# Performance work log

Hardware: AMD Instinct MI355X
Metric: run time of the kernel (lower is better)

The kernel has to match this reference:

```python
import jax, jax.numpy as jnp
import numpy as np

Q_HEADS, KV_HEADS, HEAD_SIZE, H, MAX_LEN = 16, 4, 64, 1024, 4096
B, S = 1, 4096


def _rope_tables(max_len, head_size):
    half = head_size // 2
    inv_freq = 1.0 / (10000.0 ** (np.arange(half, dtype=np.float32) / half))
    pos = np.arange(max_len, dtype=np.float32)
    ang = pos[:, None] * inv_freq[None, :]  # [max_len, half]
    return jnp.asarray(np.sin(ang)), jnp.asarray(np.cos(ang))


def setup_inputs() -> dict:
    key = jax.random.key(0)
    ks = jax.random.split(key, 6)
    sc = 1.0 / np.sqrt(H)
    x = jax.random.normal(ks[0], (B, S, H), dtype=jnp.float32)
    wq = jax.random.normal(ks[1], (H, H), dtype=jnp.float32) * sc
    wk = jax.random.normal(ks[2], (H, KV_HEADS * HEAD_SIZE), dtype=jnp.float32) * sc
    wv = jax.random.normal(ks[3], (H, KV_HEADS * HEAD_SIZE), dtype=jnp.float32) * sc
    wo = jax.random.normal(ks[4], (H, H), dtype=jnp.float32) * sc
    sin, cos = _rope_tables(MAX_LEN, HEAD_SIZE)
    full_mask = jnp.tril(jnp.ones((MAX_LEN, MAX_LEN), dtype=bool))
    attention_mask = jnp.ones((B, S), dtype=jnp.int32)
    return {"x": x, "attention_mask": attention_mask, "start": 0,
            "wq": wq, "wk": wk, "wv": wv, "wo": wo,
            "sin": sin, "cos": cos, "full_mask": full_mask}


def _rotate(t, sin, cos, start):
    # t: [b, heads, s, head_size]; interleaved even/odd RoPE
    s = t.shape[2]
    sn = sin[start:start + s, :][None, None, :, :]
    cs = cos[start:start + s, :][None, None, :, :]
    even, odd = t[..., 0::2], t[..., 1::2]
    out_even = cs * even - sn * odd
    out_odd = sn * even + cs * odd
    return jnp.stack((out_even, out_odd), axis=-1).reshape(t.shape)


def _expand_kv(t, group):
    # [b, kv_heads, s, d] -> [b, kv_heads*group, s, d]
    b, kvh, s, d = t.shape
    return jnp.broadcast_to(t[:, :, None], (b, kvh, group, s, d)).reshape(b, kvh * group, s, d)


def reference(x, attention_mask, start, wq, wk, wv, wo, sin, cos, full_mask):
    b, s, _ = x.shape
    group = Q_HEADS // KV_HEADS
    Q = (x @ wq).reshape(b, s, Q_HEADS, HEAD_SIZE).transpose(0, 2, 1, 3)
    K = (x @ wk).reshape(b, s, KV_HEADS, HEAD_SIZE).transpose(0, 2, 1, 3)
    V = (x @ wv).reshape(b, s, KV_HEADS, HEAD_SIZE).transpose(0, 2, 1, 3)
    Q = _rotate(Q, sin, cos, start)
    K = _rotate(K, sin, cos, start)
    K = _expand_kv(K, group)
    V = _expand_kv(V, group)
    z = jnp.einsum('bhqd,bhkd->bhqk', Q, K) / (HEAD_SIZE ** 0.5)
    kv_len = start + s
    mask = full_mask[:s, :kv_len][None, None, :, :]
    amask = (attention_mask[:, :kv_len] != 0)[:, None, None, :]
    mask = mask & amask
    z = jnp.where(mask, z, -1000000.0)
    A = jax.nn.softmax(z, axis=-1)
    ctx = jnp.einsum('bhqk,bhkd->bhqd', A, V)
    q_mask = attention_mask[:, :s].astype(ctx.dtype)[:, None, :, None]
    ctx = ctx * q_mask
    ctx = ctx.transpose(0, 2, 1, 3).reshape(b, s, H)
    return ctx @ wo
```

## Files before the change

### kernel.cpp

```cpp
#include <hip/hip_runtime.h>

typedef __bf16 bf16x8 __attribute__((ext_vector_type(8)));
typedef float f32x4 __attribute__((ext_vector_type(4)));
typedef unsigned int u32x4 __attribute__((ext_vector_type(4)));

typedef const void __attribute__((address_space(1)))* gas1;
typedef void __attribute__((address_space(3)))* las3;

__device__ __forceinline__ unsigned short f2bf(float f) {
  unsigned int u = __builtin_bit_cast(unsigned int, f);
  u += 0x7fffu + ((u >> 16) & 1u);
  return (unsigned short)(u >> 16);
}
__device__ __forceinline__ float bf2f(unsigned short h) {
  unsigned int u = ((unsigned int)h) << 16;
  return __builtin_bit_cast(float, u);
}
__device__ __forceinline__ unsigned int pack2bf(float lo, float hi) {
  return (unsigned int)f2bf(lo) | ((unsigned int)f2bf(hi) << 16);
}
__device__ __forceinline__ unsigned int packtr(float lo, float hi) {
  return __builtin_amdgcn_perm(__builtin_bit_cast(unsigned int, hi),
                               __builtin_bit_cast(unsigned int, lo), 0x07060302u);
}

__global__ __launch_bounds__(256) void prep(const float* __restrict__ x,
                                            const float* __restrict__ wq,
                                            const float* __restrict__ wk,
                                            const float* __restrict__ wv,
                                            const float* __restrict__ wo,
                                            const float* __restrict__ sinT,
                                            const float* __restrict__ cosT,
                                            unsigned short* __restrict__ xb,
                                            unsigned short* __restrict__ wtqkv,
                                            unsigned short* __restrict__ wot,
                                            float2* __restrict__ scT) {
  __shared__ float tile[32][33];
  const int b = blockIdx.x;
  const int tid = threadIdx.x;
  if (b < 4096) {
    int i = b * 256 + tid;
    float4 v = ((const float4*)x)[i];
    uint2 o;
    o.x = pack2bf(v.x, v.y);
    o.y = pack2bf(v.z, v.w);
    ((uint2*)xb)[i] = o;
    return;
  }
  if (b >= 6656) {
    int idx = (b - 6656) * 256 + tid;
    scT[idx] = make_float2(sinT[idx], cosT[idx]);
    return;
  }
  const float* src;
  unsigned short* dst;
  int R, C, t;
  if (b < 5120)      { t = b - 4096; src = wq; dst = wtqkv;               R = 1024; C = 1024; }
  else if (b < 5376) { t = b - 5120; src = wk; dst = wtqkv + 1024 * 1024; R = 1024; C = 256; }
  else if (b < 5632) { t = b - 5376; src = wv; dst = wtqkv + 1280 * 1024; R = 1024; C = 256; }
  else               { t = b - 5632; src = wo; dst = wot;                 R = 1024; C = 1024; }
  const int ntc = C >> 5;
  const int c0 = (t % ntc) * 32, r0 = (t / ntc) * 32;
  const int tx = tid & 31, ty = tid >> 5;
#pragma unroll
  for (int i = 0; i < 4; ++i)
    tile[ty + i * 8][tx] = src[(r0 + ty + i * 8) * C + c0 + tx];
  __syncthreads();
#pragma unroll
  for (int i = 0; i < 4; ++i)
    dst[(c0 + ty + i * 8) * R + r0 + tx] = f2bf(tile[tx][ty + i * 8]);
}


__device__ __forceinline__ void stage_tile(const unsigned short* __restrict__ src,
                                           unsigned short* lds, int tid) {
  const int w = tid >> 6;
  const int l = tid & 63;
  const int rsub = l >> 3;
  const int cblk = l & 7;
#pragma unroll
  for (int i = 0; i < 4; ++i) {
    const int row = i * 32 + w * 8 + rsub;
    const int scol = (cblk ^ (row & 7)) * 8;
    __builtin_amdgcn_global_load_lds((gas1)(const void*)&src[(size_t)row * 1024 + scol],
                                     (las3)(void*)&lds[(i * 32 + w * 8) * 64], 16, 0, 0);
  }
}

#define GEMM_STEP(CUR, NXT, KNEXT, DO_STAGE)                                          \
  {                                                                                   \
    if (DO_STAGE) {                                                                   \
      stage_tile(Ab + (KNEXT), sm[NXT][0], tid);                                      \
      stage_tile(Bb + (KNEXT), sm[NXT][1], tid);                                      \
    }                                                                                 \
    const char* As = (const char*)sm[CUR][0];                                         \
    const char* Bs = (const char*)sm[CUR][1];                                         \
    bf16x8 af[2][4], bfr[2][4];                                                       \
    _Pragma("unroll")                                                                 \
    for (int kk = 0; kk < 2; ++kk) {                                                  \
      const int co = (kk * 64 + lgrp * 16) ^ xorsel;                                  \
      _Pragma("unroll")                                                               \
      for (int mi = 0; mi < 4; ++mi)                                                  \
        af[kk][mi] = __builtin_bit_cast(bf16x8,                                       \
            *(const u32x4*)(As + arow + mi * 2048 + co));                             \
      _Pragma("unroll")                                                               \
      for (int ni = 0; ni < 4; ++ni)                                                  \
        bfr[kk][ni] = __builtin_bit_cast(bf16x8,                                      \
            *(const u32x4*)(Bs + brow + ni * 2048 + co));                             \
    }                                                                                 \
    _Pragma("unroll")                                                                 \
    for (int kk = 0; kk < 2; ++kk)                                                    \
      _Pragma("unroll")                                                               \
      for (int mi = 0; mi < 4; ++mi)                                                  \
        _Pragma("unroll")                                                             \
        for (int ni = 0; ni < 4; ++ni)                                                \
          acc[mi][ni] = __builtin_amdgcn_mfma_f32_16x16x32_bf16(af[kk][mi],           \
                            bfr[kk][ni], acc[mi][ni], 0, 0, 0);                       \
    __syncthreads();                                                                  \
  }

__global__ __launch_bounds__(256, 2) void gemm_qkv(const unsigned short* __restrict__ A,
                                                   const unsigned short* __restrict__ Bt,
                                                   const float2* __restrict__ scT,
                                                   unsigned short* __restrict__ Qh,
                                                   unsigned short* __restrict__ Kh,
                                                   unsigned short* __restrict__ Vt) {
  __shared__ __align__(16) unsigned short sm[2][2][128 * 64];
  const int tid = threadIdx.x;
  const int bid = blockIdx.x;
  const int swz = (bid & 7) * 48 + (bid >> 3);
  const int nt = swz % 12, mt = swz / 12;
  const int m0 = mt * 128, n0 = nt * 128;

  const int lane = tid & 63, wid = tid >> 6;
  const int wr = wid >> 1, wc = wid & 1;
  const int lgrp = lane >> 4, lmod = lane & 15;
  const int xorsel = (lmod & 7) << 4;
  const int arow = (wr * 64 + lmod) * 128;
  const int brow = (wc * 64 + lmod) * 128;

  const unsigned short* Ab = A + (size_t)m0 * 1024;
  const unsigned short* Bb = Bt + (size_t)n0 * 1024;

  f32x4 acc[4][4] = {};

  stage_tile(Ab, sm[0][0], tid);
  stage_tile(Bb, sm[0][1], tid);
  __syncthreads();

  for (int t = 0; t < 16; t += 2) {
    GEMM_STEP(0, 1, (size_t)(t + 1) * 64, true);
    GEMM_STEP(1, 0, (size_t)(t + 2) * 64, t < 14);
  }

  const int ncol0 = n0 + wc * 64;
  if (ncol0 >= 1280) {
    const int kvh = (ncol0 - 1280) >> 6;
#pragma unroll
    for (int mi = 0; mi < 4; ++mi)
#pragma unroll
      for (int ni = 0; ni < 4; ++ni) {
        int d = ni * 16 + lmod;
        int s = m0 + wr * 64 + mi * 16 + lgrp * 4;
        uint2 o;
        o.x = pack2bf(acc[mi][ni][0], acc[mi][ni][1]);
        o.y = pack2bf(acc[mi][ni][2], acc[mi][ni][3]);
        *(uint2*)&Vt[((size_t)(kvh * 64 + d)) * 4096 + s] = o;
      }
    return;
  }

  const float qscale = 0.18033688011112042f;
  const bool isQ = (ncol0 < 1024);
  const int h = isQ ? (ncol0 >> 6) : ((ncol0 - 1024) >> 6);
  unsigned short* dstbase = isQ ? Qh : Kh;
  const bool evn = (lmod & 1) == 0;
#pragma unroll
  for (int mi = 0; mi < 4; ++mi)
#pragma unroll
    for (int ni = 0; ni < 4; ++ni) {
      int d = ni * 16 + lmod;
      int i = d >> 1;
#pragma unroll
      for (int r = 0; r < 4; ++r) {
        float v = acc[mi][ni][r];
        float pp = __shfl_xor(v, 1, 64);
        int row = m0 + wr * 64 + mi * 16 + lgrp * 4 + r;
        float2 sc = scT[(size_t)row * 32 + i];
        float e = evn ? v : pp, o = evn ? pp : v;
        float outv = evn ? (sc.y * e - sc.x * o) : (sc.x * e + sc.y * o);
        if (isQ) outv *= qscale;
        dstbase[((size_t)h * 4096 + row) * 64 + d] = f2bf(outv);
      }
    }
}

__global__ __launch_bounds__(256, 2) void gemm_out(const unsigned short* __restrict__ A,
                                                   const unsigned short* __restrict__ Bt,
                                                   float* __restrict__ Cout) {
  __shared__ __align__(16) unsigned short sm[2][2][128 * 64];
  const int tid = threadIdx.x;
  const int bid = blockIdx.x;
  const int swz = (bid & 7) * 32 + (bid >> 3);
  const int nt = swz & 7, mt = swz >> 3;
  const int m0 = mt * 128, n0 = nt * 128;

  const int lane = tid & 63, wid = tid >> 6;
  const int wr = wid >> 1, wc = wid & 1;
  const int lgrp = lane >> 4, lmod = lane & 15;
  const int xorsel = (lmod & 7) << 4;
  const int arow = (wr * 64 + lmod) * 128;
  const int brow = (wc * 64 + lmod) * 128;

  const unsigned short* Ab = A + (size_t)m0 * 1024;
  const unsigned short* Bb = Bt + (size_t)n0 * 1024;

  f32x4 acc[4][4] = {};

  stage_tile(Ab, sm[0][0], tid);
  stage_tile(Bb, sm[0][1], tid);
  __syncthreads();

  for (int t = 0; t < 16; t += 2) {
    GEMM_STEP(0, 1, (size_t)(t + 1) * 64, true);
    GEMM_STEP(1, 0, (size_t)(t + 2) * 64, t < 14);
  }

#pragma unroll
  for (int mi = 0; mi < 4; ++mi)
#pragma unroll
    for (int ni = 0; ni < 4; ++ni)
#pragma unroll
      for (int r = 0; r < 4; ++r) {
        int row = m0 + wr * 64 + mi * 16 + lgrp * 4 + r;
        int col = n0 + wc * 64 + ni * 16 + lmod;
        Cout[(size_t)row * 1024 + col] = acc[mi][ni][r];
      }
}

__global__ __launch_bounds__(256, 2) void attn3(const unsigned short* __restrict__ Qh,
                                                const unsigned short* __restrict__ Kh,
                                                const unsigned short* __restrict__ Vt,
                                                unsigned short* __restrict__ ctx) {
  __shared__ __align__(16) unsigned short Kls[128 * 68];
  __shared__ __align__(16) unsigned short Vls[64 * 136];
  const int bx = blockIdx.x;
  const int head = bx & 15;
  const int qidx = bx >> 4;
  const int qb = (qidx < 16) ? (31 - qidx) : (qidx - 16);
  const int kvh = head >> 2;
  const int tid = threadIdx.x;
  const int wave = tid >> 6, lane = tid & 63;
  const int lgrp = lane >> 4, lmod = lane & 15;
  const int qbase = qb * 128;

  const unsigned short* Kg = Kh + (size_t)kvh * 4096 * 64;
  const unsigned short* Vg = Vt + (size_t)kvh * 64 * 4096;

  bf16x8 qf[2][2];
  int qrow[2];
#pragma unroll
  for (int qt = 0; qt < 2; ++qt) {
    qrow[qt] = qbase + wave * 32 + qt * 16 + lmod;
    const unsigned short* Qg = Qh + ((size_t)head * 4096 + qrow[qt]) * 64;
    qf[qt][0] = __builtin_bit_cast(bf16x8, *(const u32x4*)&Qg[lgrp * 8]);
    qf[qt][1] = __builtin_bit_cast(bf16x8, *(const u32x4*)&Qg[32 + lgrp * 8]);
  }

  const int kbase = (8 * (lmod >> 2) + (lmod & 3)) * 68 + lgrp * 8;
  const int vbase = lmod * 136 + lgrp * 8;

  f32x4 accO[2][4] = {};
  float m_i[2] = {-3e38f, -3e38f}, l_i[2] = {0.f, 0.f};

  for (int kc = 0; kc <= qb; ++kc) {
    const int kb = kc * 128;
    __syncthreads();
#pragma unroll
    for (int i = 0; i < 4; ++i) {
      int ii = tid + i * 256;
      int r = ii >> 3, sg = (ii & 7) * 8;
      u32x4 dK = *(const u32x4*)&Kg[(size_t)(kb + r) * 64 + sg];
      uint2* pd = (uint2*)&Kls[r * 68 + sg];
      pd[0] = make_uint2(dK[0], dK[1]);
      pd[1] = make_uint2(dK[2], dK[3]);
    }
#pragma unroll
    for (int i = 0; i < 4; ++i) {
      int ii = tid + i * 256;
      int r = ii >> 4, sg = (ii & 15) * 8;
      *(u32x4*)&Vls[r * 136 + sg] = *(const u32x4*)&Vg[(size_t)r * 4096 + kb + sg];
    }
    __syncthreads();

    f32x4 s[4][2][2];
#pragma unroll
    for (int g = 0; g < 4; ++g)
#pragma unroll
      for (int t = 0; t < 2; ++t) {
        const unsigned short* ka = &Kls[kbase + (32 * g + 4 * t) * 68];
        uint2 a0 = *(const uint2*)&ka[0];
        uint2 a1 = *(const uint2*)&ka[4];
        uint2 b0 = *(const uint2*)&ka[32];
        uint2 b1 = *(const uint2*)&ka[36];
        u32x4 lo = {a0.x, a0.y, a1.x, a1.y};
        u32x4 hi = {b0.x, b0.y, b1.x, b1.y};
        bf16x8 alo = __builtin_bit_cast(bf16x8, lo);
        bf16x8 ahi = __builtin_bit_cast(bf16x8, hi);
#pragma unroll
        for (int qt = 0; qt < 2; ++qt) {
          f32x4 z = {};
          z = __builtin_amdgcn_mfma_f32_16x16x32_bf16(alo, qf[qt][0], z, 0, 0, 0);
          z = __builtin_amdgcn_mfma_f32_16x16x32_bf16(ahi, qf[qt][1], z, 0, 0, 0);
          s[g][t][qt] = z;
        }
      }

#pragma unroll
    for (int qt = 0; qt < 2; ++qt) {
      if (kb + 127 > qbase + wave * 32 + qt * 16) {
#pragma unroll
        for (int g = 0; g < 4; ++g)
#pragma unroll
          for (int t = 0; t < 2; ++t)
#pragma unroll
            for (int r = 0; r < 4; ++r) {
              int key = kb + 32 * g + 8 * lgrp + 4 * t + r;
              if (key > qrow[qt]) s[g][t][qt][r] = -3e38f;
            }
      }
    }

#pragma unroll
    for (int qt = 0; qt < 2; ++qt) {
      f32x4 v0 = s[0][0][qt], v1 = s[0][1][qt];
#pragma unroll
      for (int g = 1; g < 4; ++g)
#pragma unroll
        for (int r = 0; r < 4; ++r) {
          v0[r] = fmaxf(v0[r], s[g][0][qt][r]);
          v1[r] = fmaxf(v1[r], s[g][1][qt][r]);
        }
      float mx = fmaxf(fmaxf(fmaxf(v0[0], v0[1]), fmaxf(v0[2], v0[3])),
                       fmaxf(fmaxf(v1[0], v1[1]), fmaxf(v1[2], v1[3])));
      mx = fmaxf(mx, __shfl_xor(mx, 16, 64));
      mx = fmaxf(mx, __shfl_xor(mx, 32, 64));
      float mnew = fmaxf(m_i[qt], mx);
      float alpha = __builtin_amdgcn_exp2f(m_i[qt] - mnew);
      m_i[qt] = mnew;
      f32x4 su = {};
#pragma unroll
      for (int g = 0; g < 4; ++g)
#pragma unroll
        for (int t = 0; t < 2; ++t)
#pragma unroll
          for (int r = 0; r < 4; ++r) {
            float ev = __builtin_amdgcn_exp2f(s[g][t][qt][r] - mnew);
            s[g][t][qt][r] = ev;
            su[r] += ev;
          }
      float rs = (su[0] + su[1]) + (su[2] + su[3]);
      rs += __shfl_xor(rs, 16, 64);
      rs += __shfl_xor(rs, 32, 64);
      l_i[qt] = l_i[qt] * alpha + rs;
#pragma unroll
      for (int dt = 0; dt < 4; ++dt)
#pragma unroll
        for (int r = 0; r < 4; ++r) accO[qt][dt][r] *= alpha;
    }

#pragma unroll
    for (int g = 0; g < 4; ++g) {
      bf16x8 pf[2];
#pragma unroll
      for (int qt = 0; qt < 2; ++qt) {
        u32x4 pk;
        pk[0] = packtr(s[g][0][qt][0], s[g][0][qt][1]);
        pk[1] = packtr(s[g][0][qt][2], s[g][0][qt][3]);
        pk[2] = packtr(s[g][1][qt][0], s[g][1][qt][1]);
        pk[3] = packtr(s[g][1][qt][2], s[g][1][qt][3]);
        pf[qt] = __builtin_bit_cast(bf16x8, pk);
      }
#pragma unroll
      for (int dt = 0; dt < 4; ++dt) {
        bf16x8 vf = __builtin_bit_cast(bf16x8, *(const u32x4*)&Vls[vbase + dt * 2176 + 32 * g]);
        accO[0][dt] = __builtin_amdgcn_mfma_f32_16x16x32_bf16(vf, pf[0], accO[0][dt], 0, 0, 0);
        accO[1][dt] = __builtin_amdgcn_mfma_f32_16x16x32_bf16(vf, pf[1], accO[1][dt], 0, 0, 0);
      }
    }
  }

#pragma unroll
  for (int qt = 0; qt < 2; ++qt) {
    float inv = 1.f / l_i[qt];
#pragma unroll
    for (int dt = 0; dt < 4; ++dt) {
      uint2 o;
      o.x = pack2bf(accO[qt][dt][0] * inv, accO[qt][dt][1] * inv);
      o.y = pack2bf(accO[qt][dt][2] * inv, accO[qt][dt][3] * inv);
      *(uint2*)&ctx[(size_t)qrow[qt] * 1024 + head * 64 + dt * 16 + lgrp * 4] = o;
    }
  }
}

extern "C" void kernel_launch(void* const* d_in, const int* in_sizes, int n_in,
                              void* d_out, int out_size, void* d_ws, size_t ws_size,
                              hipStream_t stream) {
  const float* x    = (const float*)d_in[0];
  const float* wq   = (const float*)d_in[3];
  const float* wk   = (const float*)d_in[4];
  const float* wv   = (const float*)d_in[5];
  const float* wo   = (const float*)d_in[6];
  const float* sinT = (const float*)d_in[7];
  const float* cosT = (const float*)d_in[8];

  unsigned short* ws    = (unsigned short*)d_ws;
  unsigned short* xb    = ws;
  unsigned short* wtqkv = xb + 4096 * 1024;
  unsigned short* wot   = wtqkv + 1536 * 1024;
  unsigned short* Qh    = wot + 1024 * 1024;
  unsigned short* Kh    = Qh + 16 * 4096 * 64;
  unsigned short* Vt    = Kh + 4 * 4096 * 64;
  unsigned short* ctx   = Vt + 4 * 64 * 4096;
  float2* scT           = (float2*)(ctx + 4096 * 1024);
  float* out = (float*)d_out;

  prep<<<7168, 256, 0, stream>>>(x, wq, wk, wv, wo, sinT, cosT, xb, wtqkv, wot, scT);
  gemm_qkv<<<384, 256, 0, stream>>>(xb, wtqkv, scT, Qh, Kh, Vt);
  attn3<<<dim3(512), 256, 0, stream>>>(Qh, Kh, Vt, ctx);
  gemm_out<<<256, 256, 0, stream>>>(ctx, wot, out);
}
```

Baseline: 232.9 us.

## Prefetch next K/V tile into registers and raise priority around MFMA blocks

The attention inner loop now loads the next 128-key K and V tile from global memory into registers right after the LDS barrier. Those loads overlap with the QK^T, softmax and PV compute of the current tile, and the registers are written to LDS at the start of the next iteration. It also wraps the two MFMA sections in s_setprio(1)/s_setprio(0) so waves issuing matrix ops get scheduling priority. The register prefetch adds 8 u32x4 live registers per thread, which raises register pressure and may lower occupancy.

```diff
diff --git a/kernel.cpp b/kernel.cpp
--- a/kernel.cpp
+++ b/kernel.cpp
@@ -270,30 +270,56 @@
   const int kbase = (8 * (lmod >> 2) + (lmod & 3)) * 68 + lgrp * 8;
   const int vbase = lmod * 136 + lgrp * 8;
 
+  const int krr = tid >> 3, ksg = (tid & 7) * 8;
+  const int vrr = tid >> 4, vsg = (tid & 15) * 8;
+
   f32x4 accO[2][4] = {};
   float m_i[2] = {-3e38f, -3e38f}, l_i[2] = {0.f, 0.f};
+
+  u32x4 kpre[4], vpre[4];
+#pragma unroll
+  for (int i = 0; i < 4; ++i) {
+    int r = krr + i * 32;
+    kpre[i] = *(const u32x4*)&Kg[(size_t)r * 64 + ksg];
+  }
+#pragma unroll
+  for (int i = 0; i < 4; ++i) {
+    int r = vrr + i * 16;
+    vpre[i] = *(const u32x4*)&Vg[(size_t)r * 4096 + vsg];
+  }
 
   for (int kc = 0; kc <= qb; ++kc) {
     const int kb = kc * 128;
     __syncthreads();
 #pragma unroll
     for (int i = 0; i < 4; ++i) {
-      int ii = tid + i * 256;
-      int r = ii >> 3, sg = (ii & 7) * 8;
-      u32x4 dK = *(const u32x4*)&Kg[(size_t)(kb + r) * 64 + sg];
-      uint2* pd = (uint2*)&Kls[r * 68 + sg];
-      pd[0] = make_uint2(dK[0], dK[1]);
-      pd[1] = make_uint2(dK[2], dK[3]);
+      int r = krr + i * 32;
+      uint2* pd = (uint2*)&Kls[r * 68 + ksg];
+      pd[0] = make_uint2(kpre[i][0], kpre[i][1]);
+      pd[1] = make_uint2(kpre[i][2], kpre[i][3]);
     }
 #pragma unroll
     for (int i = 0; i < 4; ++i) {
-      int ii = tid + i * 256;
-      int r = ii >> 4, sg = (ii & 15) * 8;
-      *(u32x4*)&Vls[r * 136 + sg] = *(const u32x4*)&Vg[(size_t)r * 4096 + kb + sg];
+      int r = vrr + i * 16;
+      *(u32x4*)&Vls[r * 136 + vsg] = vpre[i];
     }
     __syncthreads();
+    if (kc < qb) {
+      const int kbn = kb + 128;
+#pragma unroll
+      for (int i = 0; i < 4; ++i) {
+        int r = krr + i * 32;
+        kpre[i] = *(const u32x4*)&Kg[(size_t)(kbn + r) * 64 + ksg];
+      }
+#pragma unroll
+      for (int i = 0; i < 4; ++i) {
+        int r = vrr + i * 16;
+        vpre[i] = *(const u32x4*)&Vg[(size_t)r * 4096 + kbn + vsg];
+      }
+    }
 
     f32x4 s[4][2][2];
+    __builtin_amdgcn_s_setprio(1);
 #pragma unroll
     for (int g = 0; g < 4; ++g)
 #pragma unroll
@@ -315,6 +341,7 @@
           s[g][t][qt] = z;
         }
       }
+    __builtin_amdgcn_s_setprio(0);
 
 #pragma unroll
     for (int qt = 0; qt < 2; ++qt) {
@@ -369,6 +396,7 @@
         for (int r = 0; r < 4; ++r) accO[qt][dt][r] *= alpha;
     }
 
+    __builtin_amdgcn_s_setprio(1);
 #pragma unroll
     for (int g = 0; g < 4; ++g) {
       bf16x8 pf[2];
@@ -388,6 +416,7 @@
         accO[1][dt] = __builtin_amdgcn_mfma_f32_16x16x32_bf16(vf, pf[1], accO[1][dt], 0, 0, 0);
       }
     }
+    __builtin_amdgcn_s_setprio(0);
   }
 
 #pragma unroll
```

Result: no change. 234.1 us (+0.5%).

## Halve attention query tile to 64 rows, double grid, add MFMA priority hints

Applied to the files above, without the earlier changes.

The attention kernel now gives each block 64 query rows (16 per wave) instead of 128, doubling the grid to 1024 blocks and raising launch bounds to 4 blocks per CU. Fewer registers per thread should allow higher occupancy, and smaller work units should balance the causal triangle better. In exchange, each K/V tile loaded into LDS is reused by half as many query rows, which doubles global K/V traffic, and the last tile of each odd block is mostly masked. s_setprio hints are also added around the MFMA sections to favour matrix issue across waves.

```diff
diff --git a/kernel.cpp b/kernel.cpp
--- a/kernel.cpp
+++ b/kernel.cpp
@@ -238,7 +238,7 @@
       }
 }
 
-__global__ __launch_bounds__(256, 2) void attn3(const unsigned short* __restrict__ Qh,
+__global__ __launch_bounds__(256, 4) void attn4(const unsigned short* __restrict__ Qh,
                                                 const unsigned short* __restrict__ Kh,
                                                 const unsigned short* __restrict__ Vt,
                                                 unsigned short* __restrict__ ctx) {
@@ -247,33 +247,29 @@
   const int bx = blockIdx.x;
   const int head = bx & 15;
   const int qidx = bx >> 4;
-  const int qb = (qidx < 16) ? (31 - qidx) : (qidx - 16);
+  const int qh = (qidx < 32) ? (63 - qidx) : (qidx - 32);
   const int kvh = head >> 2;
   const int tid = threadIdx.x;
   const int wave = tid >> 6, lane = tid & 63;
   const int lgrp = lane >> 4, lmod = lane & 15;
-  const int qbase = qb * 128;
+  const int qbase = qh * 64;
+  const int ntile = qh >> 1;
 
   const unsigned short* Kg = Kh + (size_t)kvh * 4096 * 64;
   const unsigned short* Vg = Vt + (size_t)kvh * 64 * 4096;
 
-  bf16x8 qf[2][2];
-  int qrow[2];
-#pragma unroll
-  for (int qt = 0; qt < 2; ++qt) {
-    qrow[qt] = qbase + wave * 32 + qt * 16 + lmod;
-    const unsigned short* Qg = Qh + ((size_t)head * 4096 + qrow[qt]) * 64;
-    qf[qt][0] = __builtin_bit_cast(bf16x8, *(const u32x4*)&Qg[lgrp * 8]);
-    qf[qt][1] = __builtin_bit_cast(bf16x8, *(const u32x4*)&Qg[32 + lgrp * 8]);
-  }
+  const int qrow = qbase + wave * 16 + lmod;
+  const unsigned short* Qg = Qh + ((size_t)head * 4096 + qrow) * 64;
+  bf16x8 qf0 = __builtin_bit_cast(bf16x8, *(const u32x4*)&Qg[lgrp * 8]);
+  bf16x8 qf1 = __builtin_bit_cast(bf16x8, *(const u32x4*)&Qg[32 + lgrp * 8]);
 
   const int kbase = (8 * (lmod >> 2) + (lmod & 3)) * 68 + lgrp * 8;
   const int vbase = lmod * 136 + lgrp * 8;
 
-  f32x4 accO[2][4] = {};
-  float m_i[2] = {-3e38f, -3e38f}, l_i[2] = {0.f, 0.f};
-
-  for (int kc = 0; kc <= qb; ++kc) {
+  f32x4 accO[4] = {};
+  float m_i = -3e38f, l_i = 0.f;
+
+  for (int kc = 0; kc <= ntile; ++kc) {
     const int kb = kc * 128;
     __syncthreads();
 #pragma unroll
@@ -293,7 +289,8 @@
     }
     __syncthreads();
 
-    f32x4 s[4][2][2];
+    f32x4 s[4][2];
+    __builtin_amdgcn_s_setprio(1);
 #pragma unroll
     for (int g = 0; g < 4; ++g)
 #pragma unroll
@@ -307,47 +304,41 @@
         u32x4 hi = {b0.x, b0.y, b1.x, b1.y};
         bf16x8 alo = __builtin_bit_cast(bf16x8, lo);
         bf16x8 ahi = __builtin_bit_cast(bf16x8, hi);
-#pragma unroll
-        for (int qt = 0; qt < 2; ++qt) {
-          f32x4 z = {};
-          z = __builtin_amdgcn_mfma_f32_16x16x32_bf16(alo, qf[qt][0], z, 0, 0, 0);
-          z = __builtin_amdgcn_mfma_f32_16x16x32_bf16(ahi, qf[qt][1], z, 0, 0, 0);
-          s[g][t][qt] = z;
-        }
+        f32x4 z = {};
+        z = __builtin_amdgcn_mfma_f32_16x16x32_bf16(alo, qf0, z, 0, 0, 0);
+        z = __builtin_amdgcn_mfma_f32_16x16x32_bf16(ahi, qf1, z, 0, 0, 0);
+        s[g][t] = z;
       }
-
-#pragma unroll
-    for (int qt = 0; qt < 2; ++qt) {
-      if (kb + 127 > qbase + wave * 32 + qt * 16) {
-#pragma unroll
-        for (int g = 0; g < 4; ++g)
-#pragma unroll
-          for (int t = 0; t < 2; ++t)
-#pragma unroll
-            for (int r = 0; r < 4; ++r) {
-              int key = kb + 32 * g + 8 * lgrp + 4 * t + r;
-              if (key > qrow[qt]) s[g][t][qt][r] = -3e38f;
-            }
-      }
-    }
-
-#pragma unroll
-    for (int qt = 0; qt < 2; ++qt) {
-      f32x4 v0 = s[0][0][qt], v1 = s[0][1][qt];
+    __builtin_amdgcn_s_setprio(0);
+
+    if (kb + 127 > qbase + wave * 16) {
+#pragma unroll
+      for (int g = 0; g < 4; ++g)
+#pragma unroll
+        for (int t = 0; t < 2; ++t)
+#pragma unroll
+          for (int r = 0; r < 4; ++r) {
+            int key = kb + 32 * g + 8 * lgrp + 4 * t + r;
+            if (key > qrow) s[g][t][r] = -3e38f;
+          }
+    }
+
+    {
+      f32x4 v0 = s[0][0], v1 = s[0][1];
 #pragma unroll
       for (int g = 1; g < 4; ++g)
 #pragma unroll
         for (int r = 0; r < 4; ++r) {
-          v0[r] = fmaxf(v0[r], s[g][0][qt][r]);
-          v1[r] = fmaxf(v1[r], s[g][1][qt][r]);
+          v0[r] = fmaxf(v0[r], s[g][0][r]);
+          v1[r] = fmaxf(v1[r], s[g][1][r]);
         }
       float mx = fmaxf(fmaxf(fmaxf(v0[0], v0[1]), fmaxf(v0[2], v0[3])),
                        fmaxf(fmaxf(v1[0], v1[1]), fmaxf(v1[2], v1[3])));
       mx = fmaxf(mx, __shfl_xor(mx, 16, 64));
       mx = fmaxf(mx, __shfl_xor(mx, 32, 64));
-      float mnew = fmaxf(m_i[qt], mx);
-      float alpha = __builtin_amdgcn_exp2f(m_i[qt] - mnew);
-      m_i[qt] = mnew;
+      float mnew = fmaxf(m_i, mx);
+      float alpha = __builtin_amdgcn_exp2f(m_i - mnew);
+      m_i = mnew;
       f32x4 su = {};
 #pragma unroll
       for (int g = 0; g < 4; ++g)
@@ -355,50 +346,46 @@
         for (int t = 0; t < 2; ++t)
 #pragma unroll
           for (int r = 0; r < 4; ++r) {
-            float ev = __builtin_amdgcn_exp2f(s[g][t][qt][r] - mnew);
-            s[g][t][qt][r] = ev;
+            float ev = __builtin_amdgcn_exp2f(s[g][t][r] - mnew);
+            s[g][t][r] = ev;
             su[r] += ev;
           }
       float rs = (su[0] + su[1]) + (su[2] + su[3]);
       rs += __shfl_xor(rs, 16, 64);
       rs += __shfl_xor(rs, 32, 64);
-      l_i[qt] = l_i[qt] * alpha + rs;
+      l_i = l_i * alpha + rs;
 #pragma unroll
       for (int dt = 0; dt < 4; ++dt)
 #pragma unroll
-        for (int r = 0; r < 4; ++r) accO[qt][dt][r] *= alpha;
-    }
-
+        for (int r = 0; r < 4; ++r) accO[dt][r] *= alpha;
+    }
+
+    __builtin_amdgcn_s_setprio(1);
 #pragma unroll
     for (int g = 0; g < 4; ++g) {
-      bf16x8 pf[2];
-#pragma unroll
-      for (int qt = 0; qt < 2; ++qt) {
-        u32x4 pk;
-        pk[0] = packtr(s[g][0][qt][0], s[g][0][qt][1]);
-        pk[1] = packtr(s[g][0][qt][2], s[g][0][qt][3]);
-        pk[2] = packtr(s[g][1][qt][0], s[g][1][qt][1]);
-        pk[3] = packtr(s[g][1][qt][2], s[g][1][qt][3]);
-        pf[qt] = __builtin_bit_cast(bf16x8, pk);
-      }
+      u32x4 pk;
+      pk[0] = packtr(s[g][0][0], s[g][0][1]);
+      pk[1] = packtr(s[g][0][2], s[g][0][3]);
+      pk[2] = packtr(s[g][1][0], s[g][1][1]);
+      pk[3] = packtr(s[g][1][2], s[g][1][3]);
+      bf16x8 pf = __builtin_bit_cast(bf16x8, pk);
 #pragma unroll
       for (int dt = 0; dt < 4; ++dt) {
         bf16x8 vf = __builtin_bit_cast(bf16x8, *(const u32x4*)&Vls[vbase + dt * 2176 + 32 * g]);
-        accO[0][dt] = __builtin_amdgcn_mfma_f32_16x16x32_bf16(vf, pf[0], accO[0][dt], 0, 0, 0);
-        accO[1][dt] = __builtin_amdgcn_mfma_f32_16x16x32_bf16(vf, pf[1], accO[1][dt], 0, 0, 0);
+        accO[dt] = __builtin_amdgcn_mfma_f32_16x16x32_bf16(vf, pf, accO[dt], 0, 0, 0);
       }
     }
-  }
-
-#pragma unroll
-  for (int qt = 0; qt < 2; ++qt) {
-    float inv = 1.f / l_i[qt];
+    __builtin_amdgcn_s_setprio(0);
+  }
+
+  {
+    float inv = 1.f / l_i;
 #pragma unroll
     for (int dt = 0; dt < 4; ++dt) {
       uint2 o;
-      o.x = pack2bf(accO[qt][dt][0] * inv, accO[qt][dt][1] * inv);
-      o.y = pack2bf(accO[qt][dt][2] * inv, accO[qt][dt][3] * inv);
-      *(uint2*)&ctx[(size_t)qrow[qt] * 1024 + head * 64 + dt * 16 + lgrp * 4] = o;
+      o.x = pack2bf(accO[dt][0] * inv, accO[dt][1] * inv);
+      o.y = pack2bf(accO[dt][2] * inv, accO[dt][3] * inv);
+      *(uint2*)&ctx[(size_t)qrow * 1024 + head * 64 + dt * 16 + lgrp * 4] = o;
     }
   }
 }
@@ -427,6 +414,6 @@
 
   prep<<<7168, 256, 0, stream>>>(x, wq, wk, wv, wo, sinT, cosT, xb, wtqkv, wot, scT);
   gemm_qkv<<<384, 256, 0, stream>>>(xb, wtqkv, scT, Qh, Kh, Vt);
-  attn3<<<dim3(512), 256, 0, stream>>>(Qh, Kh, Vt, ctx);
+  attn4<<<dim3(1024), 256, 0, stream>>>(Qh, Kh, Vt, ctx);
   gemm_out<<<256, 256, 0, stream>>>(ctx, wot, out);
 }
```

Result: no change. 232.6 us (-0.2%).

## Shrink attention tiles to 64 queries with direct global-to-LDS swizzled loads

Applied to the files above, without the earlier changes.

The attention kernel now uses 64-row query blocks with 2 waves per block and 64-key chunks, doubling the grid to 1024 blocks for finer causal load balancing. K/V tiles are loaded with global_load_lds into an XOR-swizzled LDS layout instead of padded register-staged copies, and the key permutation inside the MFMA fragments is changed to match. MFMA sections are wrapped in s_setprio. This trades more chunk iterations, more barriers and less K/V reuse per block for higher occupancy and cheaper loads.

```diff
diff --git a/kernel.cpp b/kernel.cpp
--- a/kernel.cpp
+++ b/kernel.cpp
@@ -238,75 +238,70 @@
       }
 }
 
-__global__ __launch_bounds__(256, 2) void attn3(const unsigned short* __restrict__ Qh,
+__global__ __launch_bounds__(128, 4) void attn7(const unsigned short* __restrict__ Qh,
                                                 const unsigned short* __restrict__ Kh,
                                                 const unsigned short* __restrict__ Vt,
                                                 unsigned short* __restrict__ ctx) {
-  __shared__ __align__(16) unsigned short Kls[128 * 68];
-  __shared__ __align__(16) unsigned short Vls[64 * 136];
+  __shared__ __align__(16) unsigned short Kls[64 * 64];
+  __shared__ __align__(16) unsigned short Vls[64 * 64];
   const int bx = blockIdx.x;
   const int head = bx & 15;
   const int qidx = bx >> 4;
-  const int qb = (qidx < 16) ? (31 - qidx) : (qidx - 16);
+  const int qc = (qidx < 32) ? (63 - qidx) : (qidx - 32);
   const int kvh = head >> 2;
   const int tid = threadIdx.x;
-  const int wave = tid >> 6, lane = tid & 63;
+  const int wid = tid >> 6, lane = tid & 63;
   const int lgrp = lane >> 4, lmod = lane & 15;
-  const int qbase = qb * 128;
+  const int qbase = qc * 64;
 
   const unsigned short* Kg = Kh + (size_t)kvh * 4096 * 64;
   const unsigned short* Vg = Vt + (size_t)kvh * 64 * 4096;
 
+  int qrow[2];
   bf16x8 qf[2][2];
-  int qrow[2];
 #pragma unroll
   for (int qt = 0; qt < 2; ++qt) {
-    qrow[qt] = qbase + wave * 32 + qt * 16 + lmod;
+    qrow[qt] = qbase + wid * 32 + qt * 16 + lmod;
     const unsigned short* Qg = Qh + ((size_t)head * 4096 + qrow[qt]) * 64;
     qf[qt][0] = __builtin_bit_cast(bf16x8, *(const u32x4*)&Qg[lgrp * 8]);
     qf[qt][1] = __builtin_bit_cast(bf16x8, *(const u32x4*)&Qg[32 + lgrp * 8]);
   }
 
-  const int kbase = (8 * (lmod >> 2) + (lmod & 3)) * 68 + lgrp * 8;
-  const int vbase = lmod * 136 + lgrp * 8;
-
   f32x4 accO[2][4] = {};
   float m_i[2] = {-3e38f, -3e38f}, l_i[2] = {0.f, 0.f};
 
-  for (int kc = 0; kc <= qb; ++kc) {
-    const int kb = kc * 128;
+  for (int kc = 0; kc <= qc; ++kc) {
+    const int kb = kc * 64;
     __syncthreads();
 #pragma unroll
     for (int i = 0; i < 4; ++i) {
-      int ii = tid + i * 256;
-      int r = ii >> 3, sg = (ii & 7) * 8;
-      u32x4 dK = *(const u32x4*)&Kg[(size_t)(kb + r) * 64 + sg];
-      uint2* pd = (uint2*)&Kls[r * 68 + sg];
-      pd[0] = make_uint2(dK[0], dK[1]);
-      pd[1] = make_uint2(dK[2], dK[3]);
+      int ii = tid + i * 128;
+      int r = ii >> 3, b = ii & 7;
+      __builtin_amdgcn_global_load_lds(
+          (gas1)(const void*)&Kg[(size_t)(kb + r) * 64 + ((b ^ (r & 7)) * 8)],
+          (las3)(void*)&Kls[(size_t)ii * 8], 16, 0, 0);
     }
 #pragma unroll
     for (int i = 0; i < 4; ++i) {
-      int ii = tid + i * 256;
-      int r = ii >> 4, sg = (ii & 15) * 8;
-      *(u32x4*)&Vls[r * 136 + sg] = *(const u32x4*)&Vg[(size_t)r * 4096 + kb + sg];
+      int ii = tid + i * 128;
+      int d = ii >> 3, b = ii & 7;
+      __builtin_amdgcn_global_load_lds(
+          (gas1)(const void*)&Vg[(size_t)d * 4096 + kb + ((b ^ (d & 7)) * 8)],
+          (las3)(void*)&Vls[(size_t)ii * 8], 16, 0, 0);
     }
     __syncthreads();
 
-    f32x4 s[4][2][2];
-#pragma unroll
-    for (int g = 0; g < 4; ++g)
+    f32x4 s[2][2][2];
+    __builtin_amdgcn_s_setprio(1);
+#pragma unroll
+    for (int g = 0; g < 2; ++g)
 #pragma unroll
       for (int t = 0; t < 2; ++t) {
-        const unsigned short* ka = &Kls[kbase + (32 * g + 4 * t) * 68];
-        uint2 a0 = *(const uint2*)&ka[0];
-        uint2 a1 = *(const uint2*)&ka[4];
-        uint2 b0 = *(const uint2*)&ka[32];
-        uint2 b1 = *(const uint2*)&ka[36];
-        u32x4 lo = {a0.x, a0.y, a1.x, a1.y};
-        u32x4 hi = {b0.x, b0.y, b1.x, b1.y};
-        bf16x8 alo = __builtin_bit_cast(bf16x8, lo);
-        bf16x8 ahi = __builtin_bit_cast(bf16x8, hi);
+        const int row = 32 * g + t + 2 * lmod;
+        bf16x8 alo = __builtin_bit_cast(bf16x8,
+            *(const u32x4*)&Kls[(size_t)row * 64 + ((lgrp ^ (row & 7)) * 8)]);
+        bf16x8 ahi = __builtin_bit_cast(bf16x8,
+            *(const u32x4*)&Kls[(size_t)row * 64 + (((4 + lgrp) ^ (row & 7)) * 8)]);
 #pragma unroll
         for (int qt = 0; qt < 2; ++qt) {
           f32x4 z = {};
@@ -315,17 +310,18 @@
           s[g][t][qt] = z;
         }
       }
+    __builtin_amdgcn_s_setprio(0);
 
 #pragma unroll
     for (int qt = 0; qt < 2; ++qt) {
-      if (kb + 127 > qbase + wave * 32 + qt * 16) {
-#pragma unroll
-        for (int g = 0; g < 4; ++g)
+      if (kb + 63 > qbase + wid * 32 + qt * 16) {
+#pragma unroll
+        for (int g = 0; g < 2; ++g)
 #pragma unroll
           for (int t = 0; t < 2; ++t)
 #pragma unroll
             for (int r = 0; r < 4; ++r) {
-              int key = kb + 32 * g + 8 * lgrp + 4 * t + r;
+              int key = kb + 32 * g + 8 * lgrp + 2 * r + t;
               if (key > qrow[qt]) s[g][t][qt][r] = -3e38f;
             }
       }
@@ -335,12 +331,10 @@
     for (int qt = 0; qt < 2; ++qt) {
       f32x4 v0 = s[0][0][qt], v1 = s[0][1][qt];
 #pragma unroll
-      for (int g = 1; g < 4; ++g)
-#pragma unroll
-        for (int r = 0; r < 4; ++r) {
-          v0[r] = fmaxf(v0[r], s[g][0][qt][r]);
-          v1[r] = fmaxf(v1[r], s[g][1][qt][r]);
-        }
+      for (int r = 0; r < 4; ++r) {
+        v0[r] = fmaxf(v0[r], s[1][0][qt][r]);
+        v1[r] = fmaxf(v1[r], s[1][1][qt][r]);
+      }
       float mx = fmaxf(fmaxf(fmaxf(v0[0], v0[1]), fmaxf(v0[2], v0[3])),
                        fmaxf(fmaxf(v1[0], v1[1]), fmaxf(v1[2], v1[3])));
       mx = fmaxf(mx, __shfl_xor(mx, 16, 64));
@@ -350,7 +344,7 @@
       m_i[qt] = mnew;
       f32x4 su = {};
 #pragma unroll
-      for (int g = 0; g < 4; ++g)
+      for (int g = 0; g < 2; ++g)
 #pragma unroll
         for (int t = 0; t < 2; ++t)
 #pragma unroll
@@ -369,25 +363,29 @@
         for (int r = 0; r < 4; ++r) accO[qt][dt][r] *= alpha;
     }
 
-#pragma unroll
-    for (int g = 0; g < 4; ++g) {
+    __builtin_amdgcn_s_setprio(1);
+#pragma unroll
+    for (int g = 0; g < 2; ++g) {
       bf16x8 pf[2];
 #pragma unroll
       for (int qt = 0; qt < 2; ++qt) {
         u32x4 pk;
-        pk[0] = packtr(s[g][0][qt][0], s[g][0][qt][1]);
-        pk[1] = packtr(s[g][0][qt][2], s[g][0][qt][3]);
-        pk[2] = packtr(s[g][1][qt][0], s[g][1][qt][1]);
-        pk[3] = packtr(s[g][1][qt][2], s[g][1][qt][3]);
+        pk[0] = packtr(s[g][0][qt][0], s[g][1][qt][0]);
+        pk[1] = packtr(s[g][0][qt][1], s[g][1][qt][1]);
+        pk[2] = packtr(s[g][0][qt][2], s[g][1][qt][2]);
+        pk[3] = packtr(s[g][0][qt][3], s[g][1][qt][3]);
         pf[qt] = __builtin_bit_cast(bf16x8, pk);
       }
 #pragma unroll
       for (int dt = 0; dt < 4; ++dt) {
-        bf16x8 vf = __builtin_bit_cast(bf16x8, *(const u32x4*)&Vls[vbase + dt * 2176 + 32 * g]);
+        const int d = dt * 16 + lmod;
+        bf16x8 vf = __builtin_bit_cast(bf16x8,
+            *(const u32x4*)&Vls[(size_t)d * 64 + (((4 * g + lgrp) ^ (d & 7)) * 8)]);
         accO[0][dt] = __builtin_amdgcn_mfma_f32_16x16x32_bf16(vf, pf[0], accO[0][dt], 0, 0, 0);
         accO[1][dt] = __builtin_amdgcn_mfma_f32_16x16x32_bf16(vf, pf[1], accO[1][dt], 0, 0, 0);
       }
     }
+    __builtin_amdgcn_s_setprio(0);
   }
 
 #pragma unroll
@@ -427,6 +425,6 @@
 
   prep<<<7168, 256, 0, stream>>>(x, wq, wk, wv, wo, sinT, cosT, xb, wtqkv, wot, scT);
   gemm_qkv<<<384, 256, 0, stream>>>(xb, wtqkv, scT, Qh, Kh, Vt);
-  attn3<<<dim3(512), 256, 0, stream>>>(Qh, Kh, Vt, ctx);
+  attn7<<<dim3(1024), 128, 0, stream>>>(Qh, Kh, Vt, ctx);
   gemm_out<<<256, 256, 0, stream>>>(ctx, wot, out);
 }
```

Measured after the change: 280.9 us. 20.6% more time.
